# Kernel optimization log

Measured on AMD Instinct MI355X. Metric: run time of the kernel, lower is better.

The kernel has to match this reference:

```python
import jax, jax.numpy as jnp
import numpy as np

B, LC, LQ, D, F = 16, 2048, 256, 768, 768
MASK_VALUE = -1.0e12


def setup_inputs() -> dict:
    key = jax.random.key(0)
    ks = jax.random.split(key, 6)
    scale = 1.0 / np.sqrt(D)
    return {
        "x_cont": jax.random.normal(ks[0], (B, LC, D), dtype=jnp.float32),
        "x_ques": jax.random.normal(ks[1], (B, LQ, D), dtype=jnp.float32),
        "ques_len": jax.random.randint(ks[2], (B, 1), 0, LQ, dtype=jnp.int32),
        "WC": jax.random.normal(ks[3], (D, F), dtype=jnp.float32) * scale,
        "WQ": jax.random.normal(ks[4], (D, F), dtype=jnp.float32) * scale,
        "V": jax.random.normal(ks[5], (2 * D, F), dtype=jnp.float32) * scale,
    }


def _mask_logits(logits, ques_len):
    # Original: one_hot(ques_len[:,0], Lq) -> 1 - cumsum along Lq -> tile over Lc.
    # mask[b, j] = 1 if j < ques_len[b] else 0.
    lq = logits.shape[-1]
    oh = jax.nn.one_hot(ques_len[:, 0], lq, dtype=jnp.float32)  # [B, Lq]
    valid = 1.0 - jnp.cumsum(oh, axis=1)                         # [B, Lq]
    return logits + MASK_VALUE * (1.0 - valid)[:, None, :]       # broadcast over Lc


def reference(x_cont, x_ques, ques_len, WC, WQ, V):
    filters = WC.shape[-1]
    x_cont_ = jax.nn.relu(jnp.einsum("bcd,df->bcf", x_cont, WC))  # [B, Lc, F]
    x_ques_ = jax.nn.relu(jnp.einsum("bqd,df->bqf", x_ques, WQ))  # [B, Lq, F]
    logits = jnp.einsum("bcf,bqf->bcq", x_cont_, x_ques_) / jnp.sqrt(
        jnp.asarray(filters, dtype=x_cont.dtype)
    )  # [B, Lc, Lq]
    logits = _mask_logits(logits, ques_len)
    attn = jax.nn.softmax(logits, axis=-1)
    C = jnp.einsum("bcq,bqd->bcd", attn, x_ques)                  # [B, Lc, D]
    res = jnp.concatenate([x_cont, C], axis=2)                    # [B, Lc, 2D]
    gate = jax.nn.sigmoid(jnp.einsum("bce,ef->bcf", res, V))      # [B, Lc, F]
    return gate
```

## Files before the change

### kernel.cpp

```cpp
#include <hip/hip_runtime.h>
#include <hip/hip_bf16.h>
#include <cstdint>


using bf16 = __hip_bfloat16;
typedef __attribute__((ext_vector_type(8))) __bf16 bf16x8;
typedef __attribute__((ext_vector_type(4))) float f32x4;

typedef __attribute__((address_space(1))) const uint32_t GU32;
typedef __attribute__((address_space(3))) uint32_t LU32;

__device__ __forceinline__ void gll16(const bf16* g, bf16* l) {
  __builtin_amdgcn_global_load_lds((GU32*)g, (LU32*)l, 16, 0, 0);
}
__device__ __forceinline__ f32x4 mfma_bf16(bf16x8 a, bf16x8 b, f32x4 c) {
  return __builtin_amdgcn_mfma_f32_16x16x32_bf16(a, b, c, 0, 0, 0);
}
__device__ __forceinline__ bf16x8 ld_frag(const bf16* p) {
  return *reinterpret_cast<const bf16x8*>(p);
}
__device__ __forceinline__ int swz(int r) { return (r & 3) ^ ((r >> 2) & 1); }

__device__ __forceinline__ unsigned short f2bf_bits(float x) {
  bf16 b = __float2bfloat16(x);
  union { bf16 b; unsigned short s; } u;
  u.b = b;
  return u.s;
}

__global__ void transpose4(const float* __restrict__ s0, const float* __restrict__ s1,
                           const float* __restrict__ s2, const float* __restrict__ s3,
                           bf16* __restrict__ d0, bf16* __restrict__ d1,
                           bf16* __restrict__ d2, bf16* __restrict__ d3) {
  __shared__ float tile[32][33];
  const int z = blockIdx.z;
  const float* in = (z == 0) ? s0 : (z == 1) ? s1 : (z == 2) ? s2 : s3;
  bf16* out = (z == 0) ? d0 : (z == 1) ? d1 : (z == 2) ? d2 : d3;
  int c0 = blockIdx.x * 32, r0 = blockIdx.y * 32;
  int tx = threadIdx.x, ty = threadIdx.y;
#pragma unroll
  for (int i = ty; i < 32; i += 8)
    tile[i][tx] = in[(long)(r0 + i) * 768 + (c0 + tx)];
  __syncthreads();
#pragma unroll
  for (int i = ty; i < 32; i += 8)
    out[(long)(c0 + i) * 768 + (r0 + tx)] = __float2bfloat16(tile[tx][i]);
}

__global__ void transpose_bf16(const bf16* __restrict__ in, bf16* __restrict__ out,
                               int R, int C, long ibs, long obs) {
  __shared__ bf16 tile[32][33];
  const bf16* inb = in + (long)blockIdx.z * ibs;
  bf16* outb = out + (long)blockIdx.z * obs;
  int c0 = blockIdx.x * 32, r0 = blockIdx.y * 32;
  int tx = threadIdx.x, ty = threadIdx.y;
#pragma unroll
  for (int i = ty; i < 32; i += 8)
    tile[i][tx] = inb[(long)(r0 + i) * C + (c0 + tx)];
  __syncthreads();
#pragma unroll
  for (int i = ty; i < 32; i += 8)
    outb[(long)(c0 + i) * R + (r0 + tx)] = tile[tx][i];
}

__global__ void convert_flat(const float* __restrict__ in, bf16* __restrict__ out, long n4) {
  long i = (long)blockIdx.x * blockDim.x + threadIdx.x;
  if (i >= n4) return;
  float4 v = reinterpret_cast<const float4*>(in)[i];
  ushort4 o;
  o.x = f2bf_bits(v.x);
  o.y = f2bf_bits(v.y);
  o.z = f2bf_bits(v.z);
  o.w = f2bf_bits(v.w);
  reinterpret_cast<ushort4*>(out)[i] = o;
}

__global__ __launch_bounds__(256) void gemm_bt_split(
    const bf16* __restrict__ A, long lda,
    const bf16* __restrict__ Bt, long ldb,
    bf16* __restrict__ O1, bf16* __restrict__ O2, int K) {
  __shared__ __align__(16) bf16 As[128 * 32];
  __shared__ __align__(16) bf16 Bs[128 * 32];
  const int tid = threadIdx.x;
  const int wave = tid >> 6;
  const int lane = tid & 63;
  const int l16 = lane & 15;
  const int kh = lane >> 4;
  const int wm = (wave >> 1) * 64;
  const int wn = (wave & 1) * 64;
  const long row0 = (long)blockIdx.x * 128;
  const long col0 = (long)blockIdx.y * 128;
  const int srow = tid >> 2;
  const int scol = ((tid & 3) ^ swz(srow)) * 8;

  const bf16* ap0 = A + (row0 + srow) * lda + scol;
  const bf16* ap1 = ap0 + 64 * lda;
  const bf16* bp0 = Bt + (col0 + srow) * ldb + scol;
  const bf16* bp1 = bp0 + 64 * ldb;
  bf16* as0 = As + wave * 512;
  bf16* as1 = as0 + 2048;
  bf16* bs0 = Bs + wave * 512;
  bf16* bs1 = bs0 + 2048;

  const int xc = (kh ^ swz(l16)) * 8;
  f32x4 acc[4][4] = {};

  for (int k0 = 0; k0 < K; k0 += 32) {
    gll16(ap0 + k0, as0);
    gll16(ap1 + k0, as1);
    gll16(bp0 + k0, bs0);
    gll16(bp1 + k0, bs1);
    __syncthreads();
    bf16x8 af[4], bfr[4];
#pragma unroll
    for (int i = 0; i < 4; ++i)
      af[i] = ld_frag(As + (wm + i * 16 + l16) * 32 + xc);
#pragma unroll
    for (int j = 0; j < 4; ++j)
      bfr[j] = ld_frag(Bs + (wn + j * 16 + l16) * 32 + xc);
#pragma unroll
    for (int i = 0; i < 4; ++i)
#pragma unroll
      for (int j = 0; j < 4; ++j)
        acc[i][j] = mfma_bf16(af[i], bfr[j], acc[i][j]);
    __syncthreads();
  }

  const bool isO1 = col0 < 768;
#pragma unroll
  for (int i = 0; i < 4; ++i)
#pragma unroll
    for (int j = 0; j < 4; ++j)
#pragma unroll
      for (int r = 0; r < 4; ++r) {
        long row = row0 + wm + i * 16 + kh * 4 + r;
        long col = col0 + wn + j * 16 + l16;
        float v = acc[i][j][r];
        if (isO1)
          O1[row * 768 + col] = __float2bfloat16(fmaxf(v, 0.0f));
        else
          O2[row * 768 + (col - 768)] = __float2bfloat16(v);
      }
}

__global__ __launch_bounds__(512, 2) void gemm4b(
    const bf16* __restrict__ A, long lda,
    const bf16* __restrict__ Bt, long ldb,
    bf16* __restrict__ O1, bf16* __restrict__ O2, int K) {
  extern __shared__ __align__(16) bf16 smem[];
  const int tid = threadIdx.x;
  const int wid = tid >> 6;
  const int lane = tid & 63;
  const int l15 = lane & 15;
  const int g = lane >> 4;
  const int wm = wid >> 2;
  const int wn = wid & 3;

  const int lin = blockIdx.x;
  const int per = (int)gridDim.x >> 3;
  const int wgid = (lin & 7) * per + (lin >> 3);
  const long row0 = (long)(wgid / 6) * 256;
  const long col0 = (long)(wgid % 6) * 256;

  const int srow = lane >> 2;
  const int sc = ((lane & 3) ^ swz(srow)) * 8;
  const int w16 = wid * 16;
  const bf16* Ab = A + (row0 + srow) * lda + sc;
  const bf16* Bb = Bt + (col0 + srow) * ldb + sc;

  f32x4 acc[8][4] = {};

  auto stageA = [&](int buf, int kk) {
    bf16* d = smem + buf * 16384 + w16 * 32;
    gll16(Ab + (long)w16 * lda + kk, d);
    gll16(Ab + (long)(128 + w16) * lda + kk, d + 128 * 32);
  };
  auto stageB = [&](int buf, int kk) {
    bf16* d = smem + buf * 16384 + 8192 + w16 * 32;
    gll16(Bb + (long)w16 * ldb + kk, d);
    gll16(Bb + (long)(128 + w16) * ldb + kk, d + 128 * 32);
  };
  const int xc = (g ^ swz(l15)) * 8;
  auto ldA = [&](int buf, int m) {
    int row = wm * 128 + m * 16 + l15;
    return ld_frag(smem + buf * 16384 + row * 32 + xc);
  };
  auto ldB = [&](int buf, int n) {
    int row = wn * 64 + n * 16 + l15;
    return ld_frag(smem + buf * 16384 + 8192 + row * 32 + xc);
  };

  stageA(0, 0);
  stageB(0, 0);
  stageA(1, 32);
  stageB(1, 32);
  stageA(2, 64);
  stageB(2, 64);
  asm volatile("s_waitcnt vmcnt(8)\n\ts_barrier" ::: "memory");

  const int NT = K >> 5;
  bf16x8 av[4], bv[4];

  for (int t = 0; t < NT; ++t) {
    const int cur = t & 3;
    const int pfb = (t + 3) & 3;
    const bool pf = (t + 3) < NT;
    const int kk = (t + 3) << 5;

#pragma unroll
    for (int n = 0; n < 4; ++n) bv[n] = ldB(cur, n);
#pragma unroll
    for (int m = 0; m < 4; ++m) av[m] = ldA(cur, m);
    if (pf) stageA(pfb, kk);
    __builtin_amdgcn_s_barrier();
    __builtin_amdgcn_s_setprio(1);
#pragma unroll
    for (int m = 0; m < 4; ++m)
#pragma unroll
      for (int n = 0; n < 4; ++n) acc[m][n] = mfma_bf16(av[m], bv[n], acc[m][n]);
    __builtin_amdgcn_s_setprio(0);
    __builtin_amdgcn_s_barrier();

#pragma unroll
    for (int m = 0; m < 4; ++m) av[m] = ldA(cur, 4 + m);
    if (pf) stageB(pfb, kk);
    __builtin_amdgcn_s_barrier();
    __builtin_amdgcn_s_setprio(1);
#pragma unroll
    for (int m = 0; m < 4; ++m)
#pragma unroll
      for (int n = 0; n < 4; ++n)
        acc[4 + m][n] = mfma_bf16(av[m], bv[n], acc[4 + m][n]);
    __builtin_amdgcn_s_setprio(0);

    if (t <= NT - 4)
      asm volatile("s_waitcnt vmcnt(8)\n\ts_barrier" ::: "memory");
    else if (t == NT - 3)
      asm volatile("s_waitcnt vmcnt(4)\n\ts_barrier" ::: "memory");
    else if (t == NT - 2)
      asm volatile("s_waitcnt vmcnt(0)\n\ts_barrier" ::: "memory");
  }

  const bool isO1 = col0 < 768;
#pragma unroll
  for (int m = 0; m < 8; ++m)
#pragma unroll
    for (int n = 0; n < 4; ++n)
#pragma unroll
      for (int r = 0; r < 4; ++r) {
        long row = row0 + wm * 128 + m * 16 + g * 4 + r;
        long col = col0 + wn * 64 + n * 16 + l15;
        float v = acc[m][n][r];
        if (isO1)
          O1[row * 768 + col] = __float2bfloat16(fmaxf(v, 0.0f));
        else
          O2[row * 768 + (col - 768)] = __float2bfloat16(v);
      }
}

__global__ __launch_bounds__(512) void attn3(
    const bf16* __restrict__ xcW, const bf16* __restrict__ xqW,
    const bf16* __restrict__ xqVT, const bf16* __restrict__ G1,
    const int* __restrict__ qlen_arr, float* __restrict__ out) {
  extern __shared__ __align__(16) bf16 smem[];
  bf16* P = smem;
  float* wred = (float*)(smem + 49152);
  float* wsum = wred + 512;

  const int lin = blockIdx.x;
  const int xcd = lin & 7;
  const int jj = lin >> 3;
  const int b = xcd * 2 + (jj >> 4);
  const int ct = jj & 15;

  const int tid = threadIdx.x;
  const int wid = tid >> 6;
  const int lane = tid & 63;
  const int l16 = lane & 15;
  const int kh = lane >> 4;
  const int wm = wid >> 2;
  const int wn = wid & 3;

  const long crow0 = (long)b * 2048 + (long)ct * 128;
  const int srow = lane >> 2;
  const int sc = ((lane & 3) ^ swz(srow)) * 8;
  const int xcr = (kh ^ swz(l16)) * 8;

  const bf16* ap = xcW + (crow0 + wid * 16 + srow) * 768 + sc;
  const bf16* bp = xqW + ((long)b * 256 + wid * 32 + srow) * 768 + sc;
  const bf16* bp2 = bp + 16 * 768;

  auto stage = [&](int buf, int k0) {
    gll16(ap + k0, smem + buf * 12288 + wid * 512);
    bf16* bd = smem + buf * 12288 + 4096 + wid * 1024;
    gll16(bp + k0, bd);
    gll16(bp2 + k0, bd + 512);
  };

  f32x4 acc[4][4] = {};
  stage(0, 0);
  stage(1, 32);
  stage(2, 64);

  for (int t = 0; t < 24; ++t) {
    const int cur = t & 3;
    if (t + 3 < 24) stage((t + 3) & 3, (t + 3) * 32);
    if (t <= 20)
      asm volatile("s_waitcnt vmcnt(9)\n\ts_barrier" ::: "memory");
    else if (t == 21)
      asm volatile("s_waitcnt vmcnt(6)\n\ts_barrier" ::: "memory");
    else if (t == 22)
      asm volatile("s_waitcnt vmcnt(3)\n\ts_barrier" ::: "memory");
    else
      asm volatile("s_waitcnt vmcnt(0)\n\ts_barrier" ::: "memory");

    const bf16* Ac = smem + cur * 12288;
    const bf16* Bc = Ac + 4096;
    bf16x8 af[4], bfr[4];
#pragma unroll
    for (int i = 0; i < 4; ++i)
      af[i] = ld_frag(Ac + (wm * 64 + i * 16 + l16) * 32 + xcr);
#pragma unroll
    for (int j = 0; j < 4; ++j)
      bfr[j] = ld_frag(Bc + (wn * 64 + j * 16 + l16) * 32 + xcr);
    __builtin_amdgcn_s_setprio(1);
#pragma unroll
    for (int i = 0; i < 4; ++i)
#pragma unroll
      for (int j = 0; j < 4; ++j)
        acc[i][j] = mfma_bf16(af[i], bfr[j], acc[i][j]);
    __builtin_amdgcn_s_setprio(0);
    __builtin_amdgcn_s_barrier();
  }

  const float scale = 0.036084391824351615f;
  const int qlen = qlen_arr[b];

#pragma unroll
  for (int i = 0; i < 4; ++i)
#pragma unroll
    for (int j = 0; j < 4; ++j) {
      int col = wn * 64 + j * 16 + l16;
      float m = (col >= qlen) ? -1.0e12f : 0.0f;
#pragma unroll
      for (int r = 0; r < 4; ++r)
        acc[i][j][r] = acc[i][j][r] * scale + m;
    }

#pragma unroll
  for (int i = 0; i < 4; ++i)
#pragma unroll
    for (int r = 0; r < 4; ++r) {
      float mx = fmaxf(fmaxf(acc[i][0][r], acc[i][1][r]),
                       fmaxf(acc[i][2][r], acc[i][3][r]));
      mx = fmaxf(mx, __shfl_xor(mx, 1));
      mx = fmaxf(mx, __shfl_xor(mx, 2));
      mx = fmaxf(mx, __shfl_xor(mx, 4));
      mx = fmaxf(mx, __shfl_xor(mx, 8));
      if (l16 == 0) wred[(wm * 64 + i * 16 + kh * 4 + r) * 4 + wn] = mx;
    }
  __syncthreads();

#pragma unroll
  for (int i = 0; i < 4; ++i)
#pragma unroll
    for (int r = 0; r < 4; ++r) {
      int row = wm * 64 + i * 16 + kh * 4 + r;
      float gm = fmaxf(fmaxf(wred[row * 4 + 0], wred[row * 4 + 1]),
                       fmaxf(wred[row * 4 + 2], wred[row * 4 + 3]));
      float s = 0.0f;
#pragma unroll
      for (int j = 0; j < 4; ++j) {
        float e = expf(acc[i][j][r] - gm);
        acc[i][j][r] = e;
        s += e;
      }
      s += __shfl_xor(s, 1);
      s += __shfl_xor(s, 2);
      s += __shfl_xor(s, 4);
      s += __shfl_xor(s, 8);
      if (l16 == 0) wsum[row * 4 + wn] = s;
    }
  __syncthreads();

#pragma unroll
  for (int i = 0; i < 4; ++i)
#pragma unroll
    for (int r = 0; r < 4; ++r) {
      int row = wm * 64 + i * 16 + kh * 4 + r;
      float inv = 1.0f / (wsum[row * 4 + 0] + wsum[row * 4 + 1] +
                          wsum[row * 4 + 2] + wsum[row * 4 + 3]);
#pragma unroll
      for (int j = 0; j < 4; ++j)
        P[row * 264 + wn * 64 + j * 16 + l16] = __float2bfloat16(acc[i][j][r] * inv);
    }
  __syncthreads();

  bf16x8 pf[4][8];
#pragma unroll
  for (int i = 0; i < 4; ++i)
#pragma unroll
    for (int kk = 0; kk < 8; ++kk)
      pf[i][kk] = ld_frag(P + (wm * 64 + i * 16 + l16) * 264 + kk * 32 + kh * 8);

  for (int nb = 0; nb < 3; ++nb) {
    const int n0 = nb * 256 + wn * 64;
    const bf16* btp = xqVT + ((long)b * 768 + n0) * 256;
    f32x4 a2[4][4] = {};
#pragma unroll
    for (int kk = 0; kk < 8; ++kk) {
      bf16x8 vf[4];
#pragma unroll
      for (int j = 0; j < 4; ++j)
        vf[j] = ld_frag(btp + (j * 16 + l16) * 256 + kk * 32 + kh * 8);
#pragma unroll
      for (int i = 0; i < 4; ++i)
#pragma unroll
        for (int j = 0; j < 4; ++j)
          a2[i][j] = mfma_bf16(pf[i][kk], vf[j], a2[i][j]);
    }
#pragma unroll
    for (int i = 0; i < 4; ++i)
#pragma unroll
      for (int j = 0; j < 4; ++j)
#pragma unroll
        for (int r = 0; r < 4; ++r) {
          long row = crow0 + wm * 64 + i * 16 + kh * 4 + r;
          int col = n0 + j * 16 + l16;
          float v = a2[i][j][r] + __bfloat162float(G1[row * 768 + col]);
          out[row * 768 + col] = 1.0f / (1.0f + __expf(-v));
        }
  }
}

extern "C" void kernel_launch(void* const* d_in, const int* in_sizes, int n_in,
                              void* d_out, int out_size, void* d_ws, size_t ws_size,
                              hipStream_t stream) {
  const float* x_cont = (const float*)d_in[0];
  const float* x_ques = (const float*)d_in[1];
  const int* ques_len = (const int*)d_in[2];
  const float* WC = (const float*)d_in[3];
  const float* WQ = (const float*)d_in[4];
  const float* V = (const float*)d_in[5];
  float* out = (float*)d_out;

  bf16* Wct = (bf16*)d_ws;
  bf16* Wqt = Wct + (long)1536 * 768;
  bf16* xcB = Wqt + (long)1536 * 768;
  bf16* xqB = xcB + (long)32768 * 768;
  bf16* xcW = xqB + (long)4096 * 768;
  bf16* xqW = xcW + (long)32768 * 768;
  bf16* xqV = xqW + (long)4096 * 768;
  bf16* xqVT = xqV + (long)4096 * 768;
  bf16* G1 = xqVT + (long)16 * 768 * 256;

  (void)hipFuncSetAttribute(reinterpret_cast<const void*>(&gemm4b),
                            hipFuncAttributeMaxDynamicSharedMemorySize, 131072);
  (void)hipFuncSetAttribute(reinterpret_cast<const void*>(&attn3),
                            hipFuncAttributeMaxDynamicSharedMemorySize, 102400);

  transpose4<<<dim3(24, 24, 4), dim3(32, 8), 0, stream>>>(
      WC, WQ, V, V + (long)768 * 768,
      Wct, Wqt, Wct + (long)768 * 768, Wqt + (long)768 * 768);

  convert_flat<<<24576, 256, 0, stream>>>(x_cont, xcB, (long)32768 * 768 / 4);
  convert_flat<<<3072, 256, 0, stream>>>(x_ques, xqB, (long)4096 * 768 / 4);

  gemm_bt_split<<<dim3(32, 12), 256, 0, stream>>>(xqB, 768, Wqt, 768, xqW, xqV, 768);
  transpose_bf16<<<dim3(24, 8, 16), dim3(32, 8), 0, stream>>>(
      xqV, xqVT, 256, 768, (long)256 * 768, (long)768 * 256);

  gemm4b<<<768, 512, 131072, stream>>>(xcB, 768, Wct, 768, xcW, G1, 768);

  attn3<<<256, 512, 102400, stream>>>(xcW, xqW, xqVT, G1, ques_len, out);
}
```

Measured before the change: 248.1 us.

## Load B operand fragments directly from global into registers in GEMM and attention

The large context GEMM and the attention QK phase stop staging the B operand (weights / question projections) through LDS. Each wave now loads its B fragments straight from global memory into registers, double-buffered across k-steps, while only A is staged through LDS. The GEMM wave layout changes from 2x4 to 4x2 with 4x8 accumulators, and LDS use shrinks. The element-conversion kernel also becomes grid-stride with fewer blocks. This trades LDS traffic and footprint for more global/L2 fragment loads and higher register pressure, and relies on hand-tuned vmcnt counts staying correct.

Measured after the change: 342.4 us. +38.0%, slower.

```diff
diff --git a/kernel.cpp b/kernel.cpp
--- a/kernel.cpp
+++ b/kernel.cpp
@@ -64,15 +64,16 @@
 }
 
 __global__ void convert_flat(const float* __restrict__ in, bf16* __restrict__ out, long n4) {
-  long i = (long)blockIdx.x * blockDim.x + threadIdx.x;
-  if (i >= n4) return;
-  float4 v = reinterpret_cast<const float4*>(in)[i];
-  ushort4 o;
-  o.x = f2bf_bits(v.x);
-  o.y = f2bf_bits(v.y);
-  o.z = f2bf_bits(v.z);
-  o.w = f2bf_bits(v.w);
-  reinterpret_cast<ushort4*>(out)[i] = o;
+  long stride = (long)gridDim.x * blockDim.x;
+  for (long i = (long)blockIdx.x * blockDim.x + threadIdx.x; i < n4; i += stride) {
+    float4 v = reinterpret_cast<const float4*>(in)[i];
+    ushort4 o;
+    o.x = f2bf_bits(v.x);
+    o.y = f2bf_bits(v.y);
+    o.z = f2bf_bits(v.z);
+    o.w = f2bf_bits(v.w);
+    reinterpret_cast<ushort4*>(out)[i] = o;
+  }
 }
 
 __global__ __launch_bounds__(256) void gemm_bt_split(
@@ -143,18 +144,17 @@
       }
 }
 
-__global__ __launch_bounds__(512, 2) void gemm4b(
-    const bf16* __restrict__ A, long lda,
-    const bf16* __restrict__ Bt, long ldb,
-    bf16* __restrict__ O1, bf16* __restrict__ O2, int K) {
+__global__ __launch_bounds__(512) void gemm5(
+    const bf16* __restrict__ A, const bf16* __restrict__ Bt,
+    bf16* __restrict__ O1, bf16* __restrict__ O2) {
   extern __shared__ __align__(16) bf16 smem[];
   const int tid = threadIdx.x;
   const int wid = tid >> 6;
   const int lane = tid & 63;
-  const int l15 = lane & 15;
-  const int g = lane >> 4;
-  const int wm = wid >> 2;
-  const int wn = wid & 3;
+  const int l16 = lane & 15;
+  const int kh = lane >> 4;
+  const int wm = wid >> 1;
+  const int wn = wid & 1;
 
   const int lin = blockIdx.x;
   const int per = (int)gridDim.x >> 3;
@@ -164,92 +164,67 @@
 
   const int srow = lane >> 2;
   const int sc = ((lane & 3) ^ swz(srow)) * 8;
-  const int w16 = wid * 16;
-  const bf16* Ab = A + (row0 + srow) * lda + sc;
-  const bf16* Bb = Bt + (col0 + srow) * ldb + sc;
-
-  f32x4 acc[8][4] = {};
+  const bf16* Ab = A + (row0 + wid * 32 + srow) * 768 + sc;
+  const bf16* Bp = Bt + (col0 + wn * 128 + l16) * 768 + kh * 8;
+
+  f32x4 acc[4][8] = {};
 
   auto stageA = [&](int buf, int kk) {
-    bf16* d = smem + buf * 16384 + w16 * 32;
-    gll16(Ab + (long)w16 * lda + kk, d);
-    gll16(Ab + (long)(128 + w16) * lda + kk, d + 128 * 32);
-  };
-  auto stageB = [&](int buf, int kk) {
-    bf16* d = smem + buf * 16384 + 8192 + w16 * 32;
-    gll16(Bb + (long)w16 * ldb + kk, d);
-    gll16(Bb + (long)(128 + w16) * ldb + kk, d + 128 * 32);
-  };
-  const int xc = (g ^ swz(l15)) * 8;
-  auto ldA = [&](int buf, int m) {
-    int row = wm * 128 + m * 16 + l15;
-    return ld_frag(smem + buf * 16384 + row * 32 + xc);
-  };
-  auto ldB = [&](int buf, int n) {
-    int row = wn * 64 + n * 16 + l15;
-    return ld_frag(smem + buf * 16384 + 8192 + row * 32 + xc);
-  };
-
+    bf16* d = smem + buf * 8192 + wid * 1024;
+    gll16(Ab + kk, d);
+    gll16(Ab + 16 * 768 + kk, d + 512);
+  };
+  const int xc = (kh ^ swz(l16)) * 8;
+  auto ldA = [&](int buf, bf16x8* av) {
+#pragma unroll
+    for (int m = 0; m < 4; ++m)
+      av[m] = ld_frag(smem + buf * 8192 + (wm * 64 + m * 16 + l16) * 32 + xc);
+  };
+  auto loadB = [&](bf16x8* bv, int t) {
+#pragma unroll
+    for (int n = 0; n < 8; ++n)
+      bv[n] = ld_frag(Bp + (long)n * 16 * 768 + t * 32);
+  };
+
+  bf16x8 bvA[8], bvB[8];
+  loadB(bvA, 0);
   stageA(0, 0);
-  stageB(0, 0);
   stageA(1, 32);
-  stageB(1, 32);
   stageA(2, 64);
-  stageB(2, 64);
-  asm volatile("s_waitcnt vmcnt(8)\n\ts_barrier" ::: "memory");
-
-  const int NT = K >> 5;
-  bf16x8 av[4], bv[4];
-
-  for (int t = 0; t < NT; ++t) {
-    const int cur = t & 3;
-    const int pfb = (t + 3) & 3;
-    const bool pf = (t + 3) < NT;
-    const int kk = (t + 3) << 5;
-
-#pragma unroll
-    for (int n = 0; n < 4; ++n) bv[n] = ldB(cur, n);
-#pragma unroll
-    for (int m = 0; m < 4; ++m) av[m] = ldA(cur, m);
-    if (pf) stageA(pfb, kk);
-    __builtin_amdgcn_s_barrier();
+  asm volatile("s_waitcnt vmcnt(4)\n\ts_barrier" ::: "memory");
+
+  auto step = [&](int t, bf16x8* bc, bf16x8* bn) {
+    if (t + 1 < 24) loadB(bn, t + 1);
+    bf16x8 av[4];
+    ldA(t & 3, av);
+    if (t + 3 < 24) stageA((t + 3) & 3, (t + 3) * 32);
     __builtin_amdgcn_s_setprio(1);
 #pragma unroll
     for (int m = 0; m < 4; ++m)
 #pragma unroll
-      for (int n = 0; n < 4; ++n) acc[m][n] = mfma_bf16(av[m], bv[n], acc[m][n]);
+      for (int n = 0; n < 8; ++n)
+        acc[m][n] = mfma_bf16(av[m], bc[n], acc[m][n]);
     __builtin_amdgcn_s_setprio(0);
-    __builtin_amdgcn_s_barrier();
-
-#pragma unroll
-    for (int m = 0; m < 4; ++m) av[m] = ldA(cur, 4 + m);
-    if (pf) stageB(pfb, kk);
-    __builtin_amdgcn_s_barrier();
-    __builtin_amdgcn_s_setprio(1);
-#pragma unroll
-    for (int m = 0; m < 4; ++m)
-#pragma unroll
-      for (int n = 0; n < 4; ++n)
-        acc[4 + m][n] = mfma_bf16(av[m], bv[n], acc[4 + m][n]);
-    __builtin_amdgcn_s_setprio(0);
-
-    if (t <= NT - 4)
+    if (t < 21)
+      asm volatile("s_waitcnt vmcnt(20)\n\ts_barrier" ::: "memory");
+    else if (t < 23)
       asm volatile("s_waitcnt vmcnt(8)\n\ts_barrier" ::: "memory");
-    else if (t == NT - 3)
-      asm volatile("s_waitcnt vmcnt(4)\n\ts_barrier" ::: "memory");
-    else if (t == NT - 2)
-      asm volatile("s_waitcnt vmcnt(0)\n\ts_barrier" ::: "memory");
+  };
+
+  for (int tt = 0; tt < 12; ++tt) {
+    step(2 * tt, bvA, bvB);
+    step(2 * tt + 1, bvB, bvA);
   }
 
   const bool isO1 = col0 < 768;
 #pragma unroll
-  for (int m = 0; m < 8; ++m)
-#pragma unroll
-    for (int n = 0; n < 4; ++n)
+  for (int m = 0; m < 4; ++m)
+#pragma unroll
+    for (int n = 0; n < 8; ++n)
 #pragma unroll
       for (int r = 0; r < 4; ++r) {
-        long row = row0 + wm * 128 + m * 16 + g * 4 + r;
-        long col = col0 + wn * 64 + n * 16 + l15;
+        long row = row0 + wm * 64 + m * 16 + kh * 4 + r;
+        long col = col0 + wn * 128 + n * 16 + l16;
         float v = acc[m][n][r];
         if (isO1)
           O1[row * 768 + col] = __float2bfloat16(fmaxf(v, 0.0f));
@@ -258,13 +233,13 @@
       }
 }
 
-__global__ __launch_bounds__(512) void attn3(
+__global__ __launch_bounds__(512) void attn5(
     const bf16* __restrict__ xcW, const bf16* __restrict__ xqW,
     const bf16* __restrict__ xqVT, const bf16* __restrict__ G1,
     const int* __restrict__ qlen_arr, float* __restrict__ out) {
   extern __shared__ __align__(16) bf16 smem[];
   bf16* P = smem;
-  float* wred = (float*)(smem + 49152);
+  float* wred = (float*)(smem + 33792);
   float* wsum = wred + 512;
 
   const int lin = blockIdx.x;
@@ -287,50 +262,48 @@
   const int xcr = (kh ^ swz(l16)) * 8;
 
   const bf16* ap = xcW + (crow0 + wid * 16 + srow) * 768 + sc;
-  const bf16* bp = xqW + ((long)b * 256 + wid * 32 + srow) * 768 + sc;
-  const bf16* bp2 = bp + 16 * 768;
+  const bf16* Bp = xqW + ((long)b * 256 + wn * 64 + l16) * 768 + kh * 8;
 
   auto stage = [&](int buf, int k0) {
-    gll16(ap + k0, smem + buf * 12288 + wid * 512);
-    bf16* bd = smem + buf * 12288 + 4096 + wid * 1024;
-    gll16(bp + k0, bd);
-    gll16(bp2 + k0, bd + 512);
+    gll16(ap + k0, smem + buf * 4096 + wid * 512);
+  };
+  auto loadB = [&](bf16x8* bv, int t) {
+#pragma unroll
+    for (int j = 0; j < 4; ++j)
+      bv[j] = ld_frag(Bp + (long)j * 16 * 768 + t * 32);
   };
 
   f32x4 acc[4][4] = {};
+  bf16x8 bvA[4], bvB[4];
+  loadB(bvA, 0);
   stage(0, 0);
   stage(1, 32);
   stage(2, 64);
-
-  for (int t = 0; t < 24; ++t) {
-    const int cur = t & 3;
+  asm volatile("s_waitcnt vmcnt(2)\n\ts_barrier" ::: "memory");
+
+  auto qkstep = [&](int t, bf16x8* bc, bf16x8* bn) {
+    if (t + 1 < 24) loadB(bn, t + 1);
+    bf16x8 af[4];
+#pragma unroll
+    for (int i = 0; i < 4; ++i)
+      af[i] = ld_frag(smem + (t & 3) * 4096 + (wm * 64 + i * 16 + l16) * 32 + xcr);
     if (t + 3 < 24) stage((t + 3) & 3, (t + 3) * 32);
-    if (t <= 20)
-      asm volatile("s_waitcnt vmcnt(9)\n\ts_barrier" ::: "memory");
-    else if (t == 21)
-      asm volatile("s_waitcnt vmcnt(6)\n\ts_barrier" ::: "memory");
-    else if (t == 22)
-      asm volatile("s_waitcnt vmcnt(3)\n\ts_barrier" ::: "memory");
-    else
-      asm volatile("s_waitcnt vmcnt(0)\n\ts_barrier" ::: "memory");
-
-    const bf16* Ac = smem + cur * 12288;
-    const bf16* Bc = Ac + 4096;
-    bf16x8 af[4], bfr[4];
+    __builtin_amdgcn_s_setprio(1);
 #pragma unroll
     for (int i = 0; i < 4; ++i)
-      af[i] = ld_frag(Ac + (wm * 64 + i * 16 + l16) * 32 + xcr);
-#pragma unroll
-    for (int j = 0; j < 4; ++j)
-      bfr[j] = ld_frag(Bc + (wn * 64 + j * 16 + l16) * 32 + xcr);
-    __builtin_amdgcn_s_setprio(1);
-#pragma unroll
-    for (int i = 0; i < 4; ++i)
 #pragma unroll
       for (int j = 0; j < 4; ++j)
-        acc[i][j] = mfma_bf16(af[i], bfr[j], acc[i][j]);
+        acc[i][j] = mfma_bf16(af[i], bc[j], acc[i][j]);
     __builtin_amdgcn_s_setprio(0);
-    __builtin_amdgcn_s_barrier();
+    if (t < 21)
+      asm volatile("s_waitcnt vmcnt(10)\n\ts_barrier" ::: "memory");
+    else if (t < 23)
+      asm volatile("s_waitcnt vmcnt(4)\n\ts_barrier" ::: "memory");
+  };
+
+  for (int tt = 0; tt < 12; ++tt) {
+    qkstep(2 * tt, bvA, bvB);
+    qkstep(2 * tt + 1, bvB, bvA);
   }
 
   const float scale = 0.036084391824351615f;
@@ -454,23 +427,23 @@
   bf16* xqVT = xqV + (long)4096 * 768;
   bf16* G1 = xqVT + (long)16 * 768 * 256;
 
-  (void)hipFuncSetAttribute(reinterpret_cast<const void*>(&gemm4b),
-                            hipFuncAttributeMaxDynamicSharedMemorySize, 131072);
-  (void)hipFuncSetAttribute(reinterpret_cast<const void*>(&attn3),
-                            hipFuncAttributeMaxDynamicSharedMemorySize, 102400);
+  (void)hipFuncSetAttribute(reinterpret_cast<const void*>(&gemm5),
+                            hipFuncAttributeMaxDynamicSharedMemorySize, 65536);
+  (void)hipFuncSetAttribute(reinterpret_cast<const void*>(&attn5),
+                            hipFuncAttributeMaxDynamicSharedMemorySize, 71680);
 
   transpose4<<<dim3(24, 24, 4), dim3(32, 8), 0, stream>>>(
       WC, WQ, V, V + (long)768 * 768,
       Wct, Wqt, Wct + (long)768 * 768, Wqt + (long)768 * 768);
 
-  convert_flat<<<24576, 256, 0, stream>>>(x_cont, xcB, (long)32768 * 768 / 4);
-  convert_flat<<<3072, 256, 0, stream>>>(x_ques, xqB, (long)4096 * 768 / 4);
+  convert_flat<<<3072, 256, 0, stream>>>(x_cont, xcB, (long)32768 * 768 / 4);
+  convert_flat<<<768, 256, 0, stream>>>(x_ques, xqB, (long)4096 * 768 / 4);
 
   gemm_bt_split<<<dim3(32, 12), 256, 0, stream>>>(xqB, 768, Wqt, 768, xqW, xqV, 768);
   transpose_bf16<<<dim3(24, 8, 16), dim3(32, 8), 0, stream>>>(
       xqV, xqVT, 256, 768, (long)256 * 768, (long)768 * 256);
 
-  gemm4b<<<768, 512, 131072, stream>>>(xcB, 768, Wct, 768, xcW, G1, 768);
-
-  attn3<<<256, 512, 102400, stream>>>(xcW, xqW, xqVT, G1, ques_len, out);
-}
+  gemm5<<<768, 512, 65536, stream>>>(xcB, Wct, xcW, G1);
+
+  attn5<<<256, 512, 71680, stream>>>(xcW, xqW, xqVT, G1, ques_len, out);
+}
```

## Use 4-wave 128x128-per-wave GEMM tiles and grid-stride conversion kernels

Applied to the files above, without the earlier changes.

The main GEMM moves from 8 waves with 128x64 warp tiles to 4 waves with 128x128 warp tiles (256 threads, 1 block per CU bound), doubling per-wave accumulators and B-fragment reuse per LDS read. Each wave now stages 4 rows-of-16 per operand, and the vmcnt thresholds are adjusted to match. The fp32->bf16 conversion kernels become grid-stride loops launched with fewer blocks. The larger register footprint (256 accumulator floats per lane) risks spills and lower latency hiding with fewer waves.

Result: slower. 274.4 us (+10.6%).

```diff
diff --git a/kernel.cpp b/kernel.cpp
--- a/kernel.cpp
+++ b/kernel.cpp
@@ -64,15 +64,16 @@
 }
 
 __global__ void convert_flat(const float* __restrict__ in, bf16* __restrict__ out, long n4) {
-  long i = (long)blockIdx.x * blockDim.x + threadIdx.x;
-  if (i >= n4) return;
-  float4 v = reinterpret_cast<const float4*>(in)[i];
-  ushort4 o;
-  o.x = f2bf_bits(v.x);
-  o.y = f2bf_bits(v.y);
-  o.z = f2bf_bits(v.z);
-  o.w = f2bf_bits(v.w);
-  reinterpret_cast<ushort4*>(out)[i] = o;
+  long stride = (long)gridDim.x * blockDim.x;
+  for (long i = (long)blockIdx.x * blockDim.x + threadIdx.x; i < n4; i += stride) {
+    float4 v = reinterpret_cast<const float4*>(in)[i];
+    ushort4 o;
+    o.x = f2bf_bits(v.x);
+    o.y = f2bf_bits(v.y);
+    o.z = f2bf_bits(v.z);
+    o.w = f2bf_bits(v.w);
+    reinterpret_cast<ushort4*>(out)[i] = o;
+  }
 }
 
 __global__ __launch_bounds__(256) void gemm_bt_split(
@@ -143,7 +144,7 @@
       }
 }
 
-__global__ __launch_bounds__(512, 2) void gemm4b(
+__global__ __launch_bounds__(256, 1) void gemm6(
     const bf16* __restrict__ A, long lda,
     const bf16* __restrict__ Bt, long ldb,
     bf16* __restrict__ O1, bf16* __restrict__ O2, int K) {
@@ -151,10 +152,10 @@
   const int tid = threadIdx.x;
   const int wid = tid >> 6;
   const int lane = tid & 63;
-  const int l15 = lane & 15;
-  const int g = lane >> 4;
-  const int wm = wid >> 2;
-  const int wn = wid & 3;
+  const int l16 = lane & 15;
+  const int kh = lane >> 4;
+  const int wm = wid >> 1;
+  const int wn = wid & 1;
 
   const int lin = blockIdx.x;
   const int per = (int)gridDim.x >> 3;
@@ -164,29 +165,34 @@
 
   const int srow = lane >> 2;
   const int sc = ((lane & 3) ^ swz(srow)) * 8;
-  const int w16 = wid * 16;
   const bf16* Ab = A + (row0 + srow) * lda + sc;
   const bf16* Bb = Bt + (col0 + srow) * ldb + sc;
 
-  f32x4 acc[8][4] = {};
+  f32x4 acc[8][8] = {};
 
   auto stageA = [&](int buf, int kk) {
-    bf16* d = smem + buf * 16384 + w16 * 32;
-    gll16(Ab + (long)w16 * lda + kk, d);
-    gll16(Ab + (long)(128 + w16) * lda + kk, d + 128 * 32);
+    bf16* d = smem + buf * 16384;
+#pragma unroll
+    for (int q = 0; q < 4; ++q) {
+      int r = wid * 64 + q * 16;
+      gll16(Ab + (long)r * lda + kk, d + r * 32);
+    }
   };
   auto stageB = [&](int buf, int kk) {
-    bf16* d = smem + buf * 16384 + 8192 + w16 * 32;
-    gll16(Bb + (long)w16 * ldb + kk, d);
-    gll16(Bb + (long)(128 + w16) * ldb + kk, d + 128 * 32);
+    bf16* d = smem + buf * 16384 + 8192;
+#pragma unroll
+    for (int q = 0; q < 4; ++q) {
+      int r = wid * 64 + q * 16;
+      gll16(Bb + (long)r * ldb + kk, d + r * 32);
+    }
   };
-  const int xc = (g ^ swz(l15)) * 8;
+  const int xc = (kh ^ swz(l16)) * 8;
   auto ldA = [&](int buf, int m) {
-    int row = wm * 128 + m * 16 + l15;
+    int row = wm * 128 + m * 16 + l16;
     return ld_frag(smem + buf * 16384 + row * 32 + xc);
   };
   auto ldB = [&](int buf, int n) {
-    int row = wn * 64 + n * 16 + l15;
+    int row = wn * 128 + n * 16 + l16;
     return ld_frag(smem + buf * 16384 + 8192 + row * 32 + xc);
   };
 
@@ -196,10 +202,10 @@
   stageB(1, 32);
   stageA(2, 64);
   stageB(2, 64);
-  asm volatile("s_waitcnt vmcnt(8)\n\ts_barrier" ::: "memory");
+  asm volatile("s_waitcnt vmcnt(16)\n\ts_barrier" ::: "memory");
 
   const int NT = K >> 5;
-  bf16x8 av[4], bv[4];
+  bf16x8 av[4], bv[8];
 
   for (int t = 0; t < NT; ++t) {
     const int cur = t & 3;
@@ -208,7 +214,7 @@
     const int kk = (t + 3) << 5;
 
 #pragma unroll
-    for (int n = 0; n < 4; ++n) bv[n] = ldB(cur, n);
+    for (int n = 0; n < 8; ++n) bv[n] = ldB(cur, n);
 #pragma unroll
     for (int m = 0; m < 4; ++m) av[m] = ldA(cur, m);
     if (pf) stageA(pfb, kk);
@@ -217,7 +223,7 @@
 #pragma unroll
     for (int m = 0; m < 4; ++m)
 #pragma unroll
-      for (int n = 0; n < 4; ++n) acc[m][n] = mfma_bf16(av[m], bv[n], acc[m][n]);
+      for (int n = 0; n < 8; ++n) acc[m][n] = mfma_bf16(av[m], bv[n], acc[m][n]);
     __builtin_amdgcn_s_setprio(0);
     __builtin_amdgcn_s_barrier();
 
@@ -229,14 +235,14 @@
 #pragma unroll
     for (int m = 0; m < 4; ++m)
 #pragma unroll
-      for (int n = 0; n < 4; ++n)
+      for (int n = 0; n < 8; ++n)
         acc[4 + m][n] = mfma_bf16(av[m], bv[n], acc[4 + m][n]);
     __builtin_amdgcn_s_setprio(0);
 
     if (t <= NT - 4)
+      asm volatile("s_waitcnt vmcnt(16)\n\ts_barrier" ::: "memory");
+    else if (t == NT - 3)
       asm volatile("s_waitcnt vmcnt(8)\n\ts_barrier" ::: "memory");
-    else if (t == NT - 3)
-      asm volatile("s_waitcnt vmcnt(4)\n\ts_barrier" ::: "memory");
     else if (t == NT - 2)
       asm volatile("s_waitcnt vmcnt(0)\n\ts_barrier" ::: "memory");
   }
@@ -245,11 +251,11 @@
 #pragma unroll
   for (int m = 0; m < 8; ++m)
 #pragma unroll
-    for (int n = 0; n < 4; ++n)
+    for (int n = 0; n < 8; ++n)
 #pragma unroll
       for (int r = 0; r < 4; ++r) {
-        long row = row0 + wm * 128 + m * 16 + g * 4 + r;
-        long col = col0 + wn * 64 + n * 16 + l15;
+        long row = row0 + wm * 128 + m * 16 + kh * 4 + r;
+        long col = col0 + wn * 128 + n * 16 + l16;
         float v = acc[m][n][r];
         if (isO1)
           O1[row * 768 + col] = __float2bfloat16(fmaxf(v, 0.0f));
@@ -454,7 +460,7 @@
   bf16* xqVT = xqV + (long)4096 * 768;
   bf16* G1 = xqVT + (long)16 * 768 * 256;
 
-  (void)hipFuncSetAttribute(reinterpret_cast<const void*>(&gemm4b),
+  (void)hipFuncSetAttribute(reinterpret_cast<const void*>(&gemm6),
                             hipFuncAttributeMaxDynamicSharedMemorySize, 131072);
   (void)hipFuncSetAttribute(reinterpret_cast<const void*>(&attn3),
                             hipFuncAttributeMaxDynamicSharedMemorySize, 102400);
@@ -463,14 +469,14 @@
       WC, WQ, V, V + (long)768 * 768,
       Wct, Wqt, Wct + (long)768 * 768, Wqt + (long)768 * 768);
 
-  convert_flat<<<24576, 256, 0, stream>>>(x_cont, xcB, (long)32768 * 768 / 4);
-  convert_flat<<<3072, 256, 0, stream>>>(x_ques, xqB, (long)4096 * 768 / 4);
+  convert_flat<<<3072, 256, 0, stream>>>(x_cont, xcB, (long)32768 * 768 / 4);
+  convert_flat<<<768, 256, 0, stream>>>(x_ques, xqB, (long)4096 * 768 / 4);
 
   gemm_bt_split<<<dim3(32, 12), 256, 0, stream>>>(xqB, 768, Wqt, 768, xqW, xqV, 768);
   transpose_bf16<<<dim3(24, 8, 16), dim3(32, 8), 0, stream>>>(
       xqV, xqVT, 256, 768, (long)256 * 768, (long)768 * 256);
 
-  gemm4b<<<768, 512, 131072, stream>>>(xcB, 768, Wct, 768, xcW, G1, 768);
+  gemm6<<<768, 256, 131072, stream>>>(xcB, 768, Wct, 768, xcW, G1, 768);
 
   attn3<<<256, 512, 102400, stream>>>(xcW, xqW, xqVT, G1, ques_len, out);
 }
```

## Stage V tiles through LDS with triple-buffered async loads in attention kernel

Applied to the files above, without the earlier changes.

The P·V stage of the attention kernel now streams xqVT tiles into a three-slot LDS ring using global_load_lds, prefetching two k-steps ahead and waiting on vmcnt before each step, instead of reading fragments straight from global memory. The first tiles are issued before the softmax so the loads overlap that work, and the next block's tiles are issued after each output store. Plain __syncthreads in the softmax is replaced by a barrier that waits only on LDS counters, so the in-flight prefetches are not drained. convert_flat becomes grid-stride with fewer blocks. This adds shared memory use and extra barriers per k-step, and the hand-counted vmcnt values must match the number of outstanding loads.

Result: slower. 263.7 us (+6.3%).

```diff
diff --git a/kernel.cpp b/kernel.cpp
--- a/kernel.cpp
+++ b/kernel.cpp
@@ -26,6 +26,10 @@
   union { bf16 b; unsigned short s; } u;
   u.b = b;
   return u.s;
+}
+
+__device__ __forceinline__ void lds_barrier() {
+  asm volatile("s_waitcnt lgkmcnt(0)\n\ts_barrier" ::: "memory");
 }
 
 __global__ void transpose4(const float* __restrict__ s0, const float* __restrict__ s1,
@@ -64,15 +68,16 @@
 }
 
 __global__ void convert_flat(const float* __restrict__ in, bf16* __restrict__ out, long n4) {
-  long i = (long)blockIdx.x * blockDim.x + threadIdx.x;
-  if (i >= n4) return;
-  float4 v = reinterpret_cast<const float4*>(in)[i];
-  ushort4 o;
-  o.x = f2bf_bits(v.x);
-  o.y = f2bf_bits(v.y);
-  o.z = f2bf_bits(v.z);
-  o.w = f2bf_bits(v.w);
-  reinterpret_cast<ushort4*>(out)[i] = o;
+  long stride = (long)gridDim.x * blockDim.x;
+  for (long i = (long)blockIdx.x * blockDim.x + threadIdx.x; i < n4; i += stride) {
+    float4 v = reinterpret_cast<const float4*>(in)[i];
+    ushort4 o;
+    o.x = f2bf_bits(v.x);
+    o.y = f2bf_bits(v.y);
+    o.z = f2bf_bits(v.z);
+    o.w = f2bf_bits(v.w);
+    reinterpret_cast<ushort4*>(out)[i] = o;
+  }
 }
 
 __global__ __launch_bounds__(256) void gemm_bt_split(
@@ -258,13 +263,13 @@
       }
 }
 
-__global__ __launch_bounds__(512) void attn3(
+__global__ __launch_bounds__(512) void attn6(
     const bf16* __restrict__ xcW, const bf16* __restrict__ xqW,
     const bf16* __restrict__ xqVT, const bf16* __restrict__ G1,
     const int* __restrict__ qlen_arr, float* __restrict__ out) {
   extern __shared__ __align__(16) bf16 smem[];
-  bf16* P = smem;
-  float* wred = (float*)(smem + 49152);
+  bf16* P = smem + 24576;
+  float* wred = (float*)(smem + 58368);
   float* wsum = wred + 512;
 
   const int lin = blockIdx.x;
@@ -333,6 +338,17 @@
     __builtin_amdgcn_s_barrier();
   }
 
+  const bf16* vb = xqVT + (long)b * 768 * 256;
+  auto stage_v = [&](int nb, int kt) {
+    const bf16* src = vb + (long)(nb * 256 + wid * 32 + srow) * 256 + kt * 32 + sc;
+    bf16* d0 = smem + (kt % 3) * 8192 + (wid * 32) * 32;
+    gll16(src, d0);
+    gll16(src + 16 * 256, d0 + 512);
+  };
+
+  stage_v(0, 0);
+  stage_v(0, 1);
+
   const float scale = 0.036084391824351615f;
   const int qlen = qlen_arr[b];
 
@@ -359,7 +375,7 @@
       mx = fmaxf(mx, __shfl_xor(mx, 8));
       if (l16 == 0) wred[(wm * 64 + i * 16 + kh * 4 + r) * 4 + wn] = mx;
     }
-  __syncthreads();
+  lds_barrier();
 
 #pragma unroll
   for (int i = 0; i < 4; ++i)
@@ -381,7 +397,7 @@
       s += __shfl_xor(s, 8);
       if (l16 == 0) wsum[row * 4 + wn] = s;
     }
-  __syncthreads();
+  lds_barrier();
 
 #pragma unroll
   for (int i = 0; i < 4; ++i)
@@ -394,7 +410,7 @@
       for (int j = 0; j < 4; ++j)
         P[row * 264 + wn * 64 + j * 16 + l16] = __float2bfloat16(acc[i][j][r] * inv);
     }
-  __syncthreads();
+  lds_barrier();
 
   bf16x8 pf[4][8];
 #pragma unroll
@@ -404,21 +420,33 @@
       pf[i][kk] = ld_frag(P + (wm * 64 + i * 16 + l16) * 264 + kk * 32 + kh * 8);
 
   for (int nb = 0; nb < 3; ++nb) {
+    f32x4 a2[4][4] = {};
+#pragma unroll
+    for (int kt = 0; kt < 8; ++kt) {
+      if (kt + 2 < 8) stage_v(nb, kt + 2);
+      if (kt <= 5)
+        asm volatile("s_waitcnt vmcnt(4)\n\ts_barrier" ::: "memory");
+      else if (kt == 6)
+        asm volatile("s_waitcnt vmcnt(2)\n\ts_barrier" ::: "memory");
+      else
+        asm volatile("s_waitcnt vmcnt(0)\n\ts_barrier" ::: "memory");
+
+      const bf16* Vc = smem + (kt % 3) * 8192;
+      bf16x8 vf[4];
+#pragma unroll
+      for (int j = 0; j < 4; ++j)
+        vf[j] = ld_frag(Vc + (wn * 64 + j * 16 + l16) * 32 + xcr);
+      __builtin_amdgcn_s_setprio(1);
+#pragma unroll
+      for (int i = 0; i < 4; ++i)
+#pragma unroll
+        for (int j = 0; j < 4; ++j)
+          a2[i][j] = mfma_bf16(pf[i][kt], vf[j], a2[i][j]);
+      __builtin_amdgcn_s_setprio(0);
+      __builtin_amdgcn_s_barrier();
+    }
+
     const int n0 = nb * 256 + wn * 64;
-    const bf16* btp = xqVT + ((long)b * 768 + n0) * 256;
-    f32x4 a2[4][4] = {};
-#pragma unroll
-    for (int kk = 0; kk < 8; ++kk) {
-      bf16x8 vf[4];
-#pragma unroll
-      for (int j = 0; j < 4; ++j)
-        vf[j] = ld_frag(btp + (j * 16 + l16) * 256 + kk * 32 + kh * 8);
-#pragma unroll
-      for (int i = 0; i < 4; ++i)
-#pragma unroll
-        for (int j = 0; j < 4; ++j)
-          a2[i][j] = mfma_bf16(pf[i][kk], vf[j], a2[i][j]);
-    }
 #pragma unroll
     for (int i = 0; i < 4; ++i)
 #pragma unroll
@@ -430,6 +458,11 @@
           float v = a2[i][j][r] + __bfloat162float(G1[row * 768 + col]);
           out[row * 768 + col] = 1.0f / (1.0f + __expf(-v));
         }
+
+    if (nb + 1 < 3) {
+      stage_v(nb + 1, 0);
+      stage_v(nb + 1, 1);
+    }
   }
 }
 
@@ -456,15 +489,15 @@
 
   (void)hipFuncSetAttribute(reinterpret_cast<const void*>(&gemm4b),
                             hipFuncAttributeMaxDynamicSharedMemorySize, 131072);
-  (void)hipFuncSetAttribute(reinterpret_cast<const void*>(&attn3),
-                            hipFuncAttributeMaxDynamicSharedMemorySize, 102400);
+  (void)hipFuncSetAttribute(reinterpret_cast<const void*>(&attn6),
+                            hipFuncAttributeMaxDynamicSharedMemorySize, 120832);
 
   transpose4<<<dim3(24, 24, 4), dim3(32, 8), 0, stream>>>(
       WC, WQ, V, V + (long)768 * 768,
       Wct, Wqt, Wct + (long)768 * 768, Wqt + (long)768 * 768);
 
-  convert_flat<<<24576, 256, 0, stream>>>(x_cont, xcB, (long)32768 * 768 / 4);
-  convert_flat<<<3072, 256, 0, stream>>>(x_ques, xqB, (long)4096 * 768 / 4);
+  convert_flat<<<3072, 256, 0, stream>>>(x_cont, xcB, (long)32768 * 768 / 4);
+  convert_flat<<<768, 256, 0, stream>>>(x_ques, xqB, (long)4096 * 768 / 4);
 
   gemm_bt_split<<<dim3(32, 12), 256, 0, stream>>>(xqB, 768, Wqt, 768, xqW, xqV, 768);
   transpose_bf16<<<dim3(24, 8, 16), dim3(32, 8), 0, stream>>>(
@@ -472,5 +505,5 @@
 
   gemm4b<<<768, 512, 131072, stream>>>(xcB, 768, Wct, 768, xcW, G1, 768);
 
-  attn3<<<256, 512, 102400, stream>>>(xcW, xqW, xqVT, G1, ques_len, out);
-}
+  attn6<<<256, 512, 120832, stream>>>(xcW, xqW, xqVT, G1, ques_len, out);
+}
```
